# Kernel tuning notes

Hardware: AMD Instinct MI355X
Metric: run time of the kernel (lower is better)

## Reference

```python
import jax, jax.numpy as jnp
import numpy as np
import math

NUM_HEADS = 16
MAX_BIAS = 8.0

def _alibi_slopes(n_heads):
    def slopes(n):
        start = 2.0 ** (-2 ** (-(math.log2(n) - 3)))
        return [start * start ** i for i in range(n)]
    if math.log2(n_heads).is_integer():
        s = slopes(n_heads)
    else:
        p = 2 ** math.floor(math.log2(n_heads))
        s = slopes(p) + slopes(2 * p)[0::2][: n_heads - p]
    return jnp.asarray(np.array(s, dtype=np.float32))

def setup_inputs() -> dict:
    key = jax.random.key(0)
    ks = jax.random.split(key, 5)
    B, S, C = 2, 2048, 1024
    return {
        "x": jax.random.normal(ks[0], (B, S, C), jnp.float32),
        "in_proj_weight": jax.random.normal(ks[1], (3 * C, C), jnp.float32) * (C ** -0.5),
        "in_proj_bias": jax.random.normal(ks[2], (3 * C,), jnp.float32) * 0.02,
        "out_proj_weight": jax.random.normal(ks[3], (C, C), jnp.float32) * (C ** -0.5),
        "out_proj_bias": jax.random.normal(ks[4], (C,), jnp.float32) * 0.02,
    }

def reference(x, in_proj_weight, in_proj_bias, out_proj_weight, out_proj_bias):
    B, S, C = x.shape
    H = NUM_HEADS
    D = C // H
    # fused qkv projection: [B,S,3C] -> [3,B,H,S,D]
    qkv = x @ in_proj_weight.T + in_proj_bias
    qkv = qkv.reshape(B, S, 3, H, D).transpose(2, 0, 3, 1, 4)
    q, k, v = qkv[0], qkv[1], qkv[2]
    # ALiBi bias: slopes[h] * (i - j), clamped above at MAX_BIAS -> [H,S,S]
    slopes = _alibi_slopes(H)
    pos = jnp.arange(S, dtype=jnp.float32)
    rel = pos[:, None] - pos[None, :]  # [S,S]
    bias = jnp.minimum(rel[None, :, :] * slopes[:, None, None], MAX_BIAS)
    # scores [B,H,S,S]
    scores = jnp.einsum("bhqd,bhkd->bhqk", q, k) * (D ** -0.5) + bias[None]
    probs = jax.nn.softmax(scores, axis=-1)
    out = jnp.einsum("bhqk,bhkd->bhqd", probs, v)
    out = out.transpose(0, 2, 1, 3).reshape(B, S, C)
    return out @ out_proj_weight.T + out_proj_bias
```

## Files before the change

### kernel.cpp

```cpp
#include <hip/hip_runtime.h>
#include <hip/hip_bf16.h>

typedef __bf16 bf16;
typedef __bf16 bf16x8 __attribute__((ext_vector_type(8)));
typedef __bf16 bf16x4 __attribute__((ext_vector_type(4)));
typedef float  f32x4  __attribute__((ext_vector_type(4)));

#define LOG2E 1.44269504088896340736f


__device__ __forceinline__ void gl_lds16(const void* g, void* l) {
  __builtin_amdgcn_global_load_lds((__attribute__((address_space(1))) void*)g,
                                   (__attribute__((address_space(3))) void*)l,
                                   16, 0, 0);
}

__device__ __forceinline__ unsigned cvt_pk(float lo, float hi) {
  unsigned r;
  asm("v_cvt_pk_bf16_f32 %0, %1, %2" : "=v"(r) : "v"(lo), "v"(hi));
  return r;
}

__device__ __forceinline__ bf16x8 bits8(const unsigned* w) {
  union { unsigned u[4]; bf16x8 v; } u;
  u.u[0] = w[0]; u.u[1] = w[1]; u.u[2] = w[2]; u.u[3] = w[3];
  return u.v;
}

__global__ void cvt3_kernel(const float* __restrict__ x,
                            const float* __restrict__ w1,
                            const float* __restrict__ w2,
                            bf16* __restrict__ xb,
                            bf16* __restrict__ w1b,
                            bf16* __restrict__ w2b) {
  const int NX = 1048576, NW1 = 786432, NW2 = 262144;
  const int total = NX + NW1 + NW2;
  int i = blockIdx.x * blockDim.x + threadIdx.x;
  const int stride = gridDim.x * blockDim.x;
  for (; i < total; i += stride) {
    const float* s; bf16* d; int j;
    if (i < NX)            { s = x;  d = xb;  j = i; }
    else if (i < NX + NW1) { s = w1; d = w1b; j = i - NX; }
    else                   { s = w2; d = w2b; j = i - NX - NW1; }
    f32x4 v = ((const f32x4*)s)[j];
    bf16x4 o;
    o[0] = (bf16)v[0]; o[1] = (bf16)v[1]; o[2] = (bf16)v[2]; o[3] = (bf16)v[3];
    ((bf16x4*)d)[j] = o;
  }
}

template<int EPI>
__global__ __launch_bounds__(256) void gemm_bt(const bf16* __restrict__ A,
                                               const bf16* __restrict__ Bw,
                                               const float* __restrict__ bias,
                                               void* __restrict__ outp,
                                               int M, int N, int K) {
  __shared__ bf16 As[128 * 64];
  __shared__ bf16 Bs[128 * 64];
  const int tid  = threadIdx.x;
  const int lane = tid & 63;
  const int w    = tid >> 6;
  const int wm   = w >> 1, wn = w & 1;
  const int mBase = blockIdx.y * 128;
  const int nBase = blockIdx.x * 128;
  const int rl = lane & 15;
  const int qg = lane >> 4;
  const int srow = tid >> 3;
  const int schunk = tid & 7;

  f32x4 acc[4][4] = {};

  for (int k0 = 0; k0 < K; k0 += 64) {
    __syncthreads();
#pragma unroll
    for (int rr = 0; rr < 4; ++rr) {
      int r  = rr * 32 + srow;
      int cs = schunk ^ (r & 7);
      gl_lds16(A  + (size_t)(mBase + r) * K + k0 + cs * 8, As + r * 64 + schunk * 8);
      gl_lds16(Bw + (size_t)(nBase + r) * K + k0 + cs * 8, Bs + r * 64 + schunk * 8);
    }
    __syncthreads();
#pragma unroll
    for (int ks = 0; ks < 2; ++ks) {
      bf16x8 af[4], bfr[4];
      const int cl = ks * 4 + qg;
#pragma unroll
      for (int mf = 0; mf < 4; ++mf) {
        int r = wm * 64 + mf * 16 + rl;
        af[mf] = *(const bf16x8*)(As + r * 64 + (cl ^ (r & 7)) * 8);
      }
#pragma unroll
      for (int nf = 0; nf < 4; ++nf) {
        int r = wn * 64 + nf * 16 + rl;
        bfr[nf] = *(const bf16x8*)(Bs + r * 64 + (cl ^ (r & 7)) * 8);
      }
#pragma unroll
      for (int mf = 0; mf < 4; ++mf)
#pragma unroll
        for (int nf = 0; nf < 4; ++nf)
          acc[mf][nf] = __builtin_amdgcn_mfma_f32_16x16x32_bf16(af[mf], bfr[nf],
                                                                acc[mf][nf], 0, 0, 0);
    }
  }

#pragma unroll
  for (int mf = 0; mf < 4; ++mf) {
#pragma unroll
    for (int nf = 0; nf < 4; ++nf) {
      int n = nBase + wn * 64 + nf * 16 + rl;
      float bv = bias[n];
#pragma unroll
      for (int j = 0; j < 4; ++j) {
        int m = mBase + wm * 64 + mf * 16 + qg * 4 + j;
        float val = acc[mf][nf][j] + bv;
        if (EPI == 0) {
          int t = n >> 10, rem = n & 1023;
          int h = rem >> 6, d = rem & 63;
          int b = m >> 11, s = m & 2047;
          bf16* q = (bf16*)outp;
          size_t hb = (size_t)(b * 16 + h);
          if (t == 0) {
            q[(hb * 2048 + s) * 64 + d] = (bf16)(val * (0.125f * LOG2E));
          } else if (t == 1) {
            q[4194304 + (hb * 2048 + s) * 64 + d] = (bf16)val;
          } else {
            q[8388608 + (hb * 64 + d) * 2048 + s] = (bf16)val;
          }
        } else {
          ((float*)outp)[(size_t)m * N + n] = val;
        }
      }
    }
  }
}

__global__ __launch_bounds__(128) void attn_kernel(const bf16* __restrict__ qkv,
                                                   bf16* __restrict__ attout) {
  __shared__ bf16 Ks[64 * 64];
  __shared__ bf16 Vt[64 * 64];

  const int tid  = threadIdx.x;
  const int lane = tid & 63;
  const int w    = tid >> 6;
  const int id   = blockIdx.x;
  const int xcd  = id & 7;
  const int sel  = (id >> 3) & 1;
  const int b    = (id >> 4) & 1;
  const int qt   = 63 - (id >> 5);
  const int h    = sel ? (15 - xcd) : xcd;
  const int bh   = b * 16 + h;
  const size_t headoff = (size_t)bh * 131072;
  const bf16* Qg = qkv + headoff;
  const bf16* Kg = qkv + 4194304 + headoff;
  const bf16* Vg = qkv + 8388608 + headoff;

  const int rl = lane & 15;
  const int qg = lane >> 4;
  const int srow0  = tid >> 3;
  const int schunk = tid & 7;
  const int cs8 = (schunk ^ (srow0 & 7)) * 8;

  const int qrow = qt * 32 + w * 16 + rl;
  bf16x8 qf[2];
  qf[0] = *(const bf16x8*)(Qg + (size_t)qrow * 64 + qg * 8);
  qf[1] = *(const bf16x8*)(Qg + (size_t)qrow * 64 + 32 + qg * 8);

  bf16x8 vones;
#pragma unroll
  for (int e = 0; e < 8; ++e) vones[e] = (bf16)1.0f;

  int koff[4][2];
#pragma unroll
  for (int cf = 0; cf < 4; ++cf) {
    int r = cf * 16 + rl, r7 = r & 7;
#pragma unroll
    for (int ks = 0; ks < 2; ++ks)
      koff[cf][ks] = r * 64 + (((ks * 4 + qg) ^ r7) << 3);
  }

  const bf16* ksrc = Kg + (size_t)srow0 * 64 + cs8;
  const bf16* vsrc = Vg + (size_t)srow0 * 2048 + cs8;
  bf16* kdst = Ks + srow0 * 64 + schunk * 8;
  bf16* vdst = Vt + srow0 * 64 + schunk * 8;

  const float slope2 = exp2f(-0.5f * (float)(h + 1)) * LOG2E;
  const float nslope = -slope2;
  const float kstep  = slope2 * 64.0f;
  float basep = slope2 * (float)(qrow - qg * 4);
  float Mm    = 8.0f * LOG2E;

  const float q0f = (float)(qt * 32);
  int ktEnd = (int)floorf((q0f + 31.f + 40.f / slope2) * (1.f / 64.f)) + 1;
  if (ktEnd > 32) ktEnd = 32;
  int ktClamp = (int)floorf((q0f - 63.f - 11.6f / slope2) * (1.f / 64.f)) + 1;
  if (ktClamp < 0) ktClamp = 0;

  f32x4 o[5] = {};

  for (int kt = 0; kt < ktEnd; ++kt) {
    __syncthreads();
#pragma unroll
    for (int i = 0; i < 4; ++i)
      gl_lds16(ksrc + i * 16 * 64, kdst + i * 16 * 64);
#pragma unroll
    for (int i = 0; i < 4; ++i)
      gl_lds16(vsrc + (size_t)i * 16 * 2048, vdst + i * 16 * 64);
    ksrc += 64 * 64; vsrc += 64;
    __syncthreads();

    f32x4 sc[4] = {};
    __builtin_amdgcn_s_setprio(1);
#pragma unroll
    for (int cf = 0; cf < 4; ++cf)
#pragma unroll
      for (int ks = 0; ks < 2; ++ks) {
        bf16x8 kf = *(const bf16x8*)(Ks + koff[cf][ks]);
        sc[cf] = __builtin_amdgcn_mfma_f32_16x16x32_bf16(kf, qf[ks], sc[cf], 0, 0, 0);
      }
    __builtin_amdgcn_s_setprio(0);

    float pe[4][4];
    if (kt >= ktClamp) {
#pragma unroll
      for (int cf = 0; cf < 4; ++cf)
#pragma unroll
        for (int j = 0; j < 4; ++j)
          pe[cf][j] = sc[cf][j] +
              fminf(__builtin_fmaf(nslope, (float)(cf * 16 + j), basep), Mm);
    } else {
#pragma unroll
      for (int cf = 0; cf < 4; ++cf)
#pragma unroll
        for (int j = 0; j < 4; ++j)
          pe[cf][j] = sc[cf][j] + Mm;
    }
    float mxa = fmaxf(fmaxf(pe[0][0], pe[0][1]), fmaxf(pe[0][2], pe[0][3]));
    float mxb = fmaxf(fmaxf(pe[1][0], pe[1][1]), fmaxf(pe[1][2], pe[1][3]));
    float mxc = fmaxf(fmaxf(pe[2][0], pe[2][1]), fmaxf(pe[2][2], pe[2][3]));
    float mxd = fmaxf(fmaxf(pe[3][0], pe[3][1]), fmaxf(pe[3][2], pe[3][3]));
    float mx = fmaxf(fmaxf(mxa, mxb), fmaxf(mxc, mxd));
    mx = fmaxf(mx, __shfl_xor(mx, 16));
    mx = fmaxf(mx, __shfl_xor(mx, 32));

    if (__any(mx > 8.0f)) {
      float d = fmaxf(mx, 0.0f);
      basep -= d; Mm -= d;
      float alpha = exp2f(-d);
      float av[4];
#pragma unroll
      for (int j = 0; j < 4; ++j)
        av[j] = __shfl(alpha, qg * 4 + j);
#pragma unroll
      for (int dg = 0; dg < 5; ++dg)
#pragma unroll
        for (int j = 0; j < 4; ++j)
          o[dg][j] *= av[j];
#pragma unroll
      for (int cf = 0; cf < 4; ++cf)
#pragma unroll
        for (int j = 0; j < 4; ++j)
          pe[cf][j] = exp2f(pe[cf][j] - d);
    } else {
#pragma unroll
      for (int cf = 0; cf < 4; ++cf)
#pragma unroll
        for (int j = 0; j < 4; ++j)
          pe[cf][j] = exp2f(pe[cf][j]);
    }

    unsigned Wd[4][2];
#pragma unroll
    for (int cf = 0; cf < 4; ++cf) {
      Wd[cf][0] = cvt_pk(pe[cf][0], pe[cf][1]);
      Wd[cf][1] = cvt_pk(pe[cf][2], pe[cf][3]);
    }
    const bool hi32  = (lane & 32) != 0;
    const bool odd16 = (lane & 16) != 0;
    unsigned Aown[2], Aoth[2], Bown[2], Both[2];
#pragma unroll
    for (int u = 0; u < 2; ++u) {
      Aown[u] = hi32 ? Wd[1][u] : Wd[0][u];
      Aoth[u] = (unsigned)__shfl_xor((int)(hi32 ? Wd[0][u] : Wd[1][u]), 32);
      Bown[u] = hi32 ? Wd[3][u] : Wd[2][u];
      Both[u] = (unsigned)__shfl_xor((int)(hi32 ? Wd[2][u] : Wd[3][u]), 32);
    }
    const bool sendOwn = odd16 ^ hi32;
    unsigned fa[4], fb[4];
#pragma unroll
    for (int u = 0; u < 2; ++u) {
      unsigned rA = (unsigned)__shfl_xor((int)(sendOwn ? Aown[u] : Aoth[u]), 16);
      unsigned rB = (unsigned)__shfl_xor((int)(sendOwn ? Bown[u] : Both[u]), 16);
      fa[u]     = odd16 ? rA : (hi32 ? Aoth[u] : Aown[u]);
      fa[2 + u] = odd16 ? (hi32 ? Aown[u] : Aoth[u]) : rA;
      fb[u]     = odd16 ? rB : (hi32 ? Both[u] : Bown[u]);
      fb[2 + u] = odd16 ? (hi32 ? Bown[u] : Both[u]) : rB;
    }
    bf16x8 pa0 = bits8(fa), pa1 = bits8(fb);

    __builtin_amdgcn_s_setprio(1);
#pragma unroll
    for (int dg = 0; dg < 4; ++dg) {
      bf16x8 vb = *(const bf16x8*)(Vt + koff[dg][0]);
      o[dg] = __builtin_amdgcn_mfma_f32_16x16x32_bf16(pa0, vb, o[dg], 0, 0, 0);
    }
    o[4] = __builtin_amdgcn_mfma_f32_16x16x32_bf16(pa0, vones, o[4], 0, 0, 0);
#pragma unroll
    for (int dg = 0; dg < 4; ++dg) {
      bf16x8 vb = *(const bf16x8*)(Vt + koff[dg][1]);
      o[dg] = __builtin_amdgcn_mfma_f32_16x16x32_bf16(pa1, vb, o[dg], 0, 0, 0);
    }
    o[4] = __builtin_amdgcn_mfma_f32_16x16x32_bf16(pa1, vones, o[4], 0, 0, 0);
    __builtin_amdgcn_s_setprio(0);

    basep -= kstep;
  }

  float inv[4];
#pragma unroll
  for (int j = 0; j < 4; ++j)
    inv[j] = 1.0f / o[4][j];

#pragma unroll
  for (int dg = 0; dg < 4; ++dg)
#pragma unroll
    for (int j = 0; j < 4; ++j) {
      int row = qt * 32 + w * 16 + qg * 4 + j;
      int col = h * 64 + dg * 16 + rl;
      attout[((size_t)b * 2048 + row) * 1024 + col] = (bf16)(o[dg][j] * inv[j]);
    }
}

extern "C" void kernel_launch(void* const* d_in, const int* in_sizes, int n_in,
                              void* d_out, int out_size, void* d_ws, size_t ws_size,
                              hipStream_t stream) {
  const float* x  = (const float*)d_in[0];
  const float* w1 = (const float*)d_in[1];
  const float* b1 = (const float*)d_in[2];
  const float* w2 = (const float*)d_in[3];
  const float* b2 = (const float*)d_in[4];
  float* out = (float*)d_out;

  char* ws = (char*)d_ws;
  bf16* xb    = (bf16*)(ws);
  bf16* w1b   = (bf16*)(ws + 8388608);
  bf16* w2b   = (bf16*)(ws + 14680064);
  bf16* qkvb  = (bf16*)(ws + 16777216);
  bf16* attnb = (bf16*)(ws + 41943040);

  cvt3_kernel<<<2048, 256, 0, stream>>>(x, w1, w2, xb, w1b, w2b);
  gemm_bt<0><<<dim3(24, 32), 256, 0, stream>>>(xb, w1b, b1, (void*)qkvb, 4096, 3072, 1024);
  attn_kernel<<<2048, 128, 0, stream>>>(qkvb, attnb);
  gemm_bt<1><<<dim3(8, 32), 256, 0, stream>>>(attnb, w2b, b2, (void*)out, 4096, 1024, 1024);
}
```

Measured before the change: 190.0 us.

## Persistent attention kernel with atomic work queue and longest-first schedule

Converts the attention kernel into a persistent kernel of 768 blocks that pull work units from a global atomic counter. The counter is reset inside the conversion kernel. Units are ordered by a compile-time table that sorts (head, q-tile) pairs by how many K tiles they need, longest first. Query tiles grow from 32 to 64 rows with 256 threads per block, which halves K/V reloads per query row and is meant to reduce load imbalance from the ALiBi-based early exit. The cost is an atomic and two barriers per unit, and a possible loss of the previous XCD-aware head placement.

```diff
diff --git a/kernel.cpp b/kernel.cpp
--- a/kernel.cpp
+++ b/kernel.cpp
@@ -26,13 +26,37 @@
   u.u[0] = w[0]; u.u[1] = w[1]; u.u[2] = w[2]; u.u[3] = w[3];
   return u.v;
 }
+
+struct Sched { unsigned short u[512]; };
+constexpr Sched make_sched() {
+  Sched s{};
+  int key[512] = {};
+  for (int h = 0; h < 16; ++h) {
+    double m = 1.0;
+    for (int i = 0; i <= h; ++i) m *= 1.4142135623730951;
+    double w = 27.725887222397812 * m;
+    for (int qt = 0; qt < 32; ++qt) {
+      int ke = (int)((qt * 64.0 + 63.0 + w) / 64.0) + 1;
+      if (ke > 32) ke = 32;
+      key[h * 32 + qt] = ke;
+    }
+  }
+  int idx = 0;
+  for (int k = 32; k >= 1; --k)
+    for (int j = 0; j < 512; ++j)
+      if (key[j] == k) s.u[idx++] = (unsigned short)j;
+  return s;
+}
+__constant__ Sched SCHED = make_sched();
 
 __global__ void cvt3_kernel(const float* __restrict__ x,
                             const float* __restrict__ w1,
                             const float* __restrict__ w2,
                             bf16* __restrict__ xb,
                             bf16* __restrict__ w1b,
-                            bf16* __restrict__ w2b) {
+                            bf16* __restrict__ w2b,
+                            int* __restrict__ cnt) {
+  if (blockIdx.x == 0 && threadIdx.x == 0) *cnt = 0;
   const int NX = 1048576, NW1 = 786432, NW2 = 262144;
   const int total = NX + NW1 + NW2;
   int i = blockIdx.x * blockDim.x + threadIdx.x;
@@ -134,37 +158,22 @@
   }
 }
 
-__global__ __launch_bounds__(128) void attn_kernel(const bf16* __restrict__ qkv,
-                                                   bf16* __restrict__ attout) {
+__global__ __launch_bounds__(256) void attn_kernel(const bf16* __restrict__ qkv,
+                                                   bf16* __restrict__ attout,
+                                                   int* __restrict__ cnt) {
   __shared__ bf16 Ks[64 * 64];
   __shared__ bf16 Vt[64 * 64];
+  __shared__ int s_unit;
 
   const int tid  = threadIdx.x;
   const int lane = tid & 63;
   const int w    = tid >> 6;
-  const int id   = blockIdx.x;
-  const int xcd  = id & 7;
-  const int sel  = (id >> 3) & 1;
-  const int b    = (id >> 4) & 1;
-  const int qt   = 63 - (id >> 5);
-  const int h    = sel ? (15 - xcd) : xcd;
-  const int bh   = b * 16 + h;
-  const size_t headoff = (size_t)bh * 131072;
-  const bf16* Qg = qkv + headoff;
-  const bf16* Kg = qkv + 4194304 + headoff;
-  const bf16* Vg = qkv + 8388608 + headoff;
-
   const int rl = lane & 15;
   const int qg = lane >> 4;
   const int srow0  = tid >> 3;
   const int schunk = tid & 7;
   const int cs8 = (schunk ^ (srow0 & 7)) * 8;
 
-  const int qrow = qt * 32 + w * 16 + rl;
-  bf16x8 qf[2];
-  qf[0] = *(const bf16x8*)(Qg + (size_t)qrow * 64 + qg * 8);
-  qf[1] = *(const bf16x8*)(Qg + (size_t)qrow * 64 + 32 + qg * 8);
-
   bf16x8 vones;
 #pragma unroll
   for (int e = 0; e < 8; ++e) vones[e] = (bf16)1.0f;
@@ -177,157 +186,179 @@
     for (int ks = 0; ks < 2; ++ks)
       koff[cf][ks] = r * 64 + (((ks * 4 + qg) ^ r7) << 3);
   }
-
-  const bf16* ksrc = Kg + (size_t)srow0 * 64 + cs8;
-  const bf16* vsrc = Vg + (size_t)srow0 * 2048 + cs8;
   bf16* kdst = Ks + srow0 * 64 + schunk * 8;
   bf16* vdst = Vt + srow0 * 64 + schunk * 8;
 
-  const float slope2 = exp2f(-0.5f * (float)(h + 1)) * LOG2E;
-  const float nslope = -slope2;
-  const float kstep  = slope2 * 64.0f;
-  float basep = slope2 * (float)(qrow - qg * 4);
-  float Mm    = 8.0f * LOG2E;
-
-  const float q0f = (float)(qt * 32);
-  int ktEnd = (int)floorf((q0f + 31.f + 40.f / slope2) * (1.f / 64.f)) + 1;
-  if (ktEnd > 32) ktEnd = 32;
-  int ktClamp = (int)floorf((q0f - 63.f - 11.6f / slope2) * (1.f / 64.f)) + 1;
-  if (ktClamp < 0) ktClamp = 0;
-
-  f32x4 o[5] = {};
-
-  for (int kt = 0; kt < ktEnd; ++kt) {
+  for (;;) {
     __syncthreads();
-#pragma unroll
-    for (int i = 0; i < 4; ++i)
-      gl_lds16(ksrc + i * 16 * 64, kdst + i * 16 * 64);
-#pragma unroll
-    for (int i = 0; i < 4; ++i)
-      gl_lds16(vsrc + (size_t)i * 16 * 2048, vdst + i * 16 * 64);
-    ksrc += 64 * 64; vsrc += 64;
+    if (tid == 0) s_unit = atomicAdd(cnt, 1);
     __syncthreads();
-
-    f32x4 sc[4] = {};
-    __builtin_amdgcn_s_setprio(1);
-#pragma unroll
-    for (int cf = 0; cf < 4; ++cf)
-#pragma unroll
-      for (int ks = 0; ks < 2; ++ks) {
-        bf16x8 kf = *(const bf16x8*)(Ks + koff[cf][ks]);
-        sc[cf] = __builtin_amdgcn_mfma_f32_16x16x32_bf16(kf, qf[ks], sc[cf], 0, 0, 0);
-      }
-    __builtin_amdgcn_s_setprio(0);
-
-    float pe[4][4];
-    if (kt >= ktClamp) {
+    const int unit = s_unit;
+    if (unit >= 1024) return;
+
+    const int e  = SCHED.u[unit >> 1];
+    const int b  = unit & 1;
+    const int h  = e >> 5;
+    const int qt = e & 31;
+    const int bh = b * 16 + h;
+    const size_t headoff = (size_t)bh * 131072;
+    const bf16* Qg = qkv + headoff;
+    const bf16* Kg = qkv + 4194304 + headoff;
+    const bf16* Vg = qkv + 8388608 + headoff;
+
+    const int qrow = qt * 64 + w * 16 + rl;
+    bf16x8 qf[2];
+    qf[0] = *(const bf16x8*)(Qg + (size_t)qrow * 64 + qg * 8);
+    qf[1] = *(const bf16x8*)(Qg + (size_t)qrow * 64 + 32 + qg * 8);
+
+    const bf16* ksrc = Kg + (size_t)srow0 * 64 + cs8;
+    const bf16* vsrc = Vg + (size_t)srow0 * 2048 + cs8;
+
+    const float slope2 = exp2f(-0.5f * (float)(h + 1)) * LOG2E;
+    const float nslope = -slope2;
+    const float kstep  = slope2 * 64.0f;
+    float basep = slope2 * (float)(qrow - qg * 4);
+    float Mm    = 8.0f * LOG2E;
+
+    const float q0f = (float)(qt * 64);
+    int ktEnd = (int)floorf((q0f + 63.f + 40.f / slope2) * (1.f / 64.f)) + 1;
+    if (ktEnd > 32) ktEnd = 32;
+    int ktClamp = (int)floorf((q0f - 63.f - 11.6f / slope2) * (1.f / 64.f)) + 1;
+    if (ktClamp < 0) ktClamp = 0;
+
+    f32x4 o[5] = {};
+
+    for (int kt = 0; kt < ktEnd; ++kt) {
+      __syncthreads();
+#pragma unroll
+      for (int i = 0; i < 2; ++i) {
+        gl_lds16(ksrc + i * 32 * 64,          kdst + i * 32 * 64);
+        gl_lds16(vsrc + (size_t)i * 32 * 2048, vdst + i * 32 * 64);
+      }
+      ksrc += 64 * 64; vsrc += 64;
+      __syncthreads();
+
+      f32x4 sc[4] = {};
+      __builtin_amdgcn_s_setprio(1);
 #pragma unroll
       for (int cf = 0; cf < 4; ++cf)
 #pragma unroll
+        for (int ks = 0; ks < 2; ++ks) {
+          bf16x8 kf = *(const bf16x8*)(Ks + koff[cf][ks]);
+          sc[cf] = __builtin_amdgcn_mfma_f32_16x16x32_bf16(kf, qf[ks], sc[cf], 0, 0, 0);
+        }
+      __builtin_amdgcn_s_setprio(0);
+
+      float pe[4][4];
+      if (kt >= ktClamp) {
+#pragma unroll
+        for (int cf = 0; cf < 4; ++cf)
+#pragma unroll
+          for (int j = 0; j < 4; ++j)
+            pe[cf][j] = sc[cf][j] +
+                fminf(__builtin_fmaf(nslope, (float)(cf * 16 + j), basep), Mm);
+      } else {
+#pragma unroll
+        for (int cf = 0; cf < 4; ++cf)
+#pragma unroll
+          for (int j = 0; j < 4; ++j)
+            pe[cf][j] = sc[cf][j] + Mm;
+      }
+      float mxa = fmaxf(fmaxf(pe[0][0], pe[0][1]), fmaxf(pe[0][2], pe[0][3]));
+      float mxb = fmaxf(fmaxf(pe[1][0], pe[1][1]), fmaxf(pe[1][2], pe[1][3]));
+      float mxc = fmaxf(fmaxf(pe[2][0], pe[2][1]), fmaxf(pe[2][2], pe[2][3]));
+      float mxd = fmaxf(fmaxf(pe[3][0], pe[3][1]), fmaxf(pe[3][2], pe[3][3]));
+      float mx = fmaxf(fmaxf(mxa, mxb), fmaxf(mxc, mxd));
+      mx = fmaxf(mx, __shfl_xor(mx, 16));
+      mx = fmaxf(mx, __shfl_xor(mx, 32));
+
+      if (__any(mx > 8.0f)) {
+        float d = fmaxf(mx, 0.0f);
+        basep -= d; Mm -= d;
+        float alpha = exp2f(-d);
+        float av[4];
+#pragma unroll
         for (int j = 0; j < 4; ++j)
-          pe[cf][j] = sc[cf][j] +
-              fminf(__builtin_fmaf(nslope, (float)(cf * 16 + j), basep), Mm);
-    } else {
-#pragma unroll
-      for (int cf = 0; cf < 4; ++cf)
-#pragma unroll
-        for (int j = 0; j < 4; ++j)
-          pe[cf][j] = sc[cf][j] + Mm;
-    }
-    float mxa = fmaxf(fmaxf(pe[0][0], pe[0][1]), fmaxf(pe[0][2], pe[0][3]));
-    float mxb = fmaxf(fmaxf(pe[1][0], pe[1][1]), fmaxf(pe[1][2], pe[1][3]));
-    float mxc = fmaxf(fmaxf(pe[2][0], pe[2][1]), fmaxf(pe[2][2], pe[2][3]));
-    float mxd = fmaxf(fmaxf(pe[3][0], pe[3][1]), fmaxf(pe[3][2], pe[3][3]));
-    float mx = fmaxf(fmaxf(mxa, mxb), fmaxf(mxc, mxd));
-    mx = fmaxf(mx, __shfl_xor(mx, 16));
-    mx = fmaxf(mx, __shfl_xor(mx, 32));
-
-    if (__any(mx > 8.0f)) {
-      float d = fmaxf(mx, 0.0f);
-      basep -= d; Mm -= d;
-      float alpha = exp2f(-d);
-      float av[4];
-#pragma unroll
-      for (int j = 0; j < 4; ++j)
-        av[j] = __shfl(alpha, qg * 4 + j);
-#pragma unroll
-      for (int dg = 0; dg < 5; ++dg)
-#pragma unroll
-        for (int j = 0; j < 4; ++j)
-          o[dg][j] *= av[j];
-#pragma unroll
-      for (int cf = 0; cf < 4; ++cf)
-#pragma unroll
-        for (int j = 0; j < 4; ++j)
-          pe[cf][j] = exp2f(pe[cf][j] - d);
-    } else {
-#pragma unroll
-      for (int cf = 0; cf < 4; ++cf)
-#pragma unroll
-        for (int j = 0; j < 4; ++j)
-          pe[cf][j] = exp2f(pe[cf][j]);
-    }
-
-    unsigned Wd[4][2];
-#pragma unroll
-    for (int cf = 0; cf < 4; ++cf) {
-      Wd[cf][0] = cvt_pk(pe[cf][0], pe[cf][1]);
-      Wd[cf][1] = cvt_pk(pe[cf][2], pe[cf][3]);
-    }
-    const bool hi32  = (lane & 32) != 0;
-    const bool odd16 = (lane & 16) != 0;
-    unsigned Aown[2], Aoth[2], Bown[2], Both[2];
-#pragma unroll
-    for (int u = 0; u < 2; ++u) {
-      Aown[u] = hi32 ? Wd[1][u] : Wd[0][u];
-      Aoth[u] = (unsigned)__shfl_xor((int)(hi32 ? Wd[0][u] : Wd[1][u]), 32);
-      Bown[u] = hi32 ? Wd[3][u] : Wd[2][u];
-      Both[u] = (unsigned)__shfl_xor((int)(hi32 ? Wd[2][u] : Wd[3][u]), 32);
-    }
-    const bool sendOwn = odd16 ^ hi32;
-    unsigned fa[4], fb[4];
-#pragma unroll
-    for (int u = 0; u < 2; ++u) {
-      unsigned rA = (unsigned)__shfl_xor((int)(sendOwn ? Aown[u] : Aoth[u]), 16);
-      unsigned rB = (unsigned)__shfl_xor((int)(sendOwn ? Bown[u] : Both[u]), 16);
-      fa[u]     = odd16 ? rA : (hi32 ? Aoth[u] : Aown[u]);
-      fa[2 + u] = odd16 ? (hi32 ? Aown[u] : Aoth[u]) : rA;
-      fb[u]     = odd16 ? rB : (hi32 ? Both[u] : Bown[u]);
-      fb[2 + u] = odd16 ? (hi32 ? Bown[u] : Both[u]) : rB;
-    }
-    bf16x8 pa0 = bits8(fa), pa1 = bits8(fb);
-
-    __builtin_amdgcn_s_setprio(1);
-#pragma unroll
-    for (int dg = 0; dg < 4; ++dg) {
-      bf16x8 vb = *(const bf16x8*)(Vt + koff[dg][0]);
-      o[dg] = __builtin_amdgcn_mfma_f32_16x16x32_bf16(pa0, vb, o[dg], 0, 0, 0);
-    }
-    o[4] = __builtin_amdgcn_mfma_f32_16x16x32_bf16(pa0, vones, o[4], 0, 0, 0);
-#pragma unroll
-    for (int dg = 0; dg < 4; ++dg) {
-      bf16x8 vb = *(const bf16x8*)(Vt + koff[dg][1]);
-      o[dg] = __builtin_amdgcn_mfma_f32_16x16x32_bf16(pa1, vb, o[dg], 0, 0, 0);
-    }
-    o[4] = __builtin_amdgcn_mfma_f32_16x16x32_bf16(pa1, vones, o[4], 0, 0, 0);
-    __builtin_amdgcn_s_setprio(0);
-
-    basep -= kstep;
-  }
-
-  float inv[4];
-#pragma unroll
-  for (int j = 0; j < 4; ++j)
-    inv[j] = 1.0f / o[4][j];
-
-#pragma unroll
-  for (int dg = 0; dg < 4; ++dg)
-#pragma unroll
-    for (int j = 0; j < 4; ++j) {
-      int row = qt * 32 + w * 16 + qg * 4 + j;
-      int col = h * 64 + dg * 16 + rl;
-      attout[((size_t)b * 2048 + row) * 1024 + col] = (bf16)(o[dg][j] * inv[j]);
-    }
+          av[j] = __shfl(alpha, qg * 4 + j);
+#pragma unroll
+        for (int dg = 0; dg < 5; ++dg)
+#pragma unroll
+          for (int j = 0; j < 4; ++j)
+            o[dg][j] *= av[j];
+#pragma unroll
+        for (int cf = 0; cf < 4; ++cf)
+#pragma unroll
+          for (int j = 0; j < 4; ++j)
+            pe[cf][j] = exp2f(pe[cf][j] - d);
+      } else {
+#pragma unroll
+        for (int cf = 0; cf < 4; ++cf)
+#pragma unroll
+          for (int j = 0; j < 4; ++j)
+            pe[cf][j] = exp2f(pe[cf][j]);
+      }
+
+      unsigned Wd[4][2];
+#pragma unroll
+      for (int cf = 0; cf < 4; ++cf) {
+        Wd[cf][0] = cvt_pk(pe[cf][0], pe[cf][1]);
+        Wd[cf][1] = cvt_pk(pe[cf][2], pe[cf][3]);
+      }
+      const bool hi32  = (lane & 32) != 0;
+      const bool odd16 = (lane & 16) != 0;
+      unsigned Aown[2], Aoth[2], Bown[2], Both[2];
+#pragma unroll
+      for (int u = 0; u < 2; ++u) {
+        Aown[u] = hi32 ? Wd[1][u] : Wd[0][u];
+        Aoth[u] = (unsigned)__shfl_xor((int)(hi32 ? Wd[0][u] : Wd[1][u]), 32);
+        Bown[u] = hi32 ? Wd[3][u] : Wd[2][u];
+        Both[u] = (unsigned)__shfl_xor((int)(hi32 ? Wd[2][u] : Wd[3][u]), 32);
+      }
+      const bool sendOwn = odd16 ^ hi32;
+      unsigned fa[4], fb[4];
+#pragma unroll
+      for (int u = 0; u < 2; ++u) {
+        unsigned rA = (unsigned)__shfl_xor((int)(sendOwn ? Aown[u] : Aoth[u]), 16);
+        unsigned rB = (unsigned)__shfl_xor((int)(sendOwn ? Bown[u] : Both[u]), 16);
+        fa[u]     = odd16 ? rA : (hi32 ? Aoth[u] : Aown[u]);
+        fa[2 + u] = odd16 ? (hi32 ? Aown[u] : Aoth[u]) : rA;
+        fb[u]     = odd16 ? rB : (hi32 ? Both[u] : Bown[u]);
+        fb[2 + u] = odd16 ? (hi32 ? Bown[u] : Both[u]) : rB;
+      }
+      bf16x8 pa0 = bits8(fa), pa1 = bits8(fb);
+
+      __builtin_amdgcn_s_setprio(1);
+#pragma unroll
+      for (int dg = 0; dg < 4; ++dg) {
+        bf16x8 vb = *(const bf16x8*)(Vt + koff[dg][0]);
+        o[dg] = __builtin_amdgcn_mfma_f32_16x16x32_bf16(pa0, vb, o[dg], 0, 0, 0);
+      }
+      o[4] = __builtin_amdgcn_mfma_f32_16x16x32_bf16(pa0, vones, o[4], 0, 0, 0);
+#pragma unroll
+      for (int dg = 0; dg < 4; ++dg) {
+        bf16x8 vb = *(const bf16x8*)(Vt + koff[dg][1]);
+        o[dg] = __builtin_amdgcn_mfma_f32_16x16x32_bf16(pa1, vb, o[dg], 0, 0, 0);
+      }
+      o[4] = __builtin_amdgcn_mfma_f32_16x16x32_bf16(pa1, vones, o[4], 0, 0, 0);
+      __builtin_amdgcn_s_setprio(0);
+
+      basep -= kstep;
+    }
+
+    float inv[4];
+#pragma unroll
+    for (int j = 0; j < 4; ++j)
+      inv[j] = 1.0f / o[4][j];
+
+#pragma unroll
+    for (int dg = 0; dg < 4; ++dg)
+#pragma unroll
+      for (int j = 0; j < 4; ++j) {
+        int row = qt * 64 + w * 16 + qg * 4 + j;
+        int col = h * 64 + dg * 16 + rl;
+        attout[((size_t)b * 2048 + row) * 1024 + col] = (bf16)(o[dg][j] * inv[j]);
+      }
+  }
 }
 
 extern "C" void kernel_launch(void* const* d_in, const int* in_sizes, int n_in,
@@ -341,14 +372,15 @@
   float* out = (float*)d_out;
 
   char* ws = (char*)d_ws;
-  bf16* xb    = (bf16*)(ws);
-  bf16* w1b   = (bf16*)(ws + 8388608);
-  bf16* w2b   = (bf16*)(ws + 14680064);
-  bf16* qkvb  = (bf16*)(ws + 16777216);
-  bf16* attnb = (bf16*)(ws + 41943040);
-
-  cvt3_kernel<<<2048, 256, 0, stream>>>(x, w1, w2, xb, w1b, w2b);
+  int*  cnt   = (int*)(ws);
+  bf16* xb    = (bf16*)(ws + 16);
+  bf16* w1b   = (bf16*)(ws + 8388608 + 16);
+  bf16* w2b   = (bf16*)(ws + 14680064 + 16);
+  bf16* qkvb  = (bf16*)(ws + 16777216 + 16);
+  bf16* attnb = (bf16*)(ws + 41943040 + 16);
+
+  cvt3_kernel<<<2048, 256, 0, stream>>>(x, w1, w2, xb, w1b, w2b, cnt);
   gemm_bt<0><<<dim3(24, 32), 256, 0, stream>>>(xb, w1b, b1, (void*)qkvb, 4096, 3072, 1024);
-  attn_kernel<<<2048, 128, 0, stream>>>(qkvb, attnb);
+  attn_kernel<<<768, 256, 0, stream>>>(qkvb, attnb, cnt);
   gemm_bt<1><<<dim3(8, 32), 256, 0, stream>>>(attnb, w2b, b2, (void*)out, 4096, 1024, 1024);
 }
```

New measurement: 170.9 us. 10.0% less time.
